# Kernel tuning notes

Hardware: AMD Instinct MI355X
Metric: run time of the kernel (lower is better)

## Reference

```python
import jax, jax.numpy as jnp
import numpy as np

DIM_SINGLE = 384
DIM_PAIR = 128
HEADS = 12
DIM_POINT = 4
B, N = 1, 1024
EPS = 1e-5


def _gram_schmidt_rot(key, shape):
    k1, k2 = jax.random.split(key)
    v1 = jax.random.normal(k1, shape + (3,), jnp.float32)
    v2 = jax.random.normal(k2, shape + (3,), jnp.float32)
    x = v1 / jnp.linalg.norm(v1, axis=-1, keepdims=True)
    z = jnp.cross(x, v2)
    z = z / jnp.linalg.norm(z, axis=-1, keepdims=True)
    y = jnp.cross(z, x)
    # columns are basis vectors, matching torch.stack([x,y,z], dim=-1)
    return jnp.stack([x, y, z], axis=-1)


def setup_inputs() -> dict:
    key = jax.random.key(0)
    ks = jax.random.split(key, 24)
    C, Cp, H, P = DIM_SINGLE, DIM_PAIR, HEADS, DIM_POINT
    HP3 = H * P * 3
    s = lambda k, sh, sc: (jax.random.normal(k, sh, jnp.float32) * sc)
    inp = {
        'single': jax.random.normal(ks[0], (B, N, C), jnp.float32),
        'pair': jax.random.normal(ks[1], (B, N, N, Cp), jnp.float32),
        'rot': _gram_schmidt_rot(ks[2], (B, N)),
        'trans': jax.random.normal(ks[3], (B, N, 3), jnp.float32),
        'mask': jnp.ones((B, N), dtype=bool),
        'Wq': s(ks[4], (C, C), C ** -0.5), 'bq': jnp.zeros((C,), jnp.float32),
        'Wk': s(ks[5], (C, C), C ** -0.5), 'bk': jnp.zeros((C,), jnp.float32),
        'Wv': s(ks[6], (C, C), C ** -0.5), 'bv': jnp.zeros((C,), jnp.float32),
        'Wpb': s(ks[7], (Cp, H), Cp ** -0.5), 'bpb': jnp.zeros((H,), jnp.float32),
        'Wqp': s(ks[8], (C, HP3), C ** -0.5), 'bqp': jnp.zeros((HP3,), jnp.float32),
        'Wkp': s(ks[9], (C, HP3), C ** -0.5), 'bkp': jnp.zeros((HP3,), jnp.float32),
        'Wvp': s(ks[10], (C, HP3), C ** -0.5), 'bvp': jnp.zeros((HP3,), jnp.float32),
        'Wo': s(ks[11], (C, C), C ** -0.5), 'bo': jnp.zeros((C,), jnp.float32),
        'Wpo': s(ks[12], (HP3, C), HP3 ** -0.5), 'bpo': jnp.zeros((C,), jnp.float32),
        'gamma': jnp.ones((C,), jnp.float32), 'beta': jnp.zeros((C,), jnp.float32),
    }
    return inp


def ipa_forward(single, pair, rot, trans, mask,
                Wq, bq, Wk, bk, Wv, bv, Wpb, bpb,
                Wqp, bqp, Wkp, bkp, Wvp, bvp,
                Wo, bo, Wpo, bpo, gamma, beta):
    Bn, Nn, C = single.shape
    H, P = HEADS, DIM_POINT
    Ch = C // H
    scale = Ch ** -0.5

    q = (single @ Wq + bq).reshape(Bn, Nn, H, Ch)
    k = (single @ Wk + bk).reshape(Bn, Nn, H, Ch)
    v = (single @ Wv + bv).reshape(Bn, Nn, H, Ch)

    pair_bias = (pair @ Wpb + bpb).transpose(0, 3, 1, 2)  # [B,H,N,N]

    def pts(W, b):
        p = (single @ W + b).reshape(Bn, Nn, H, P, 3)
        # point as row-vector times rot (matches torch einsum bnhpd,bnhde->bnhpe)
        p = jnp.einsum('bnhpd,bnde->bnhpe', p, rot) + trans[:, :, None, None, :]
        return p

    q_pts = pts(Wqp, bqp)
    k_pts = pts(Wkp, bkp)
    v_pts = pts(Wvp, bvp)

    q2 = jnp.sum(q_pts ** 2, axis=(3, 4))  # [B,N,H]
    k2 = jnp.sum(k_pts ** 2, axis=(3, 4))

    scalar_logits = jnp.einsum('bmhc,bnhc->bhmn', q, k) * scale
    qk_pts = jnp.einsum('bmhpd,bnhpd->bhmn', q_pts, k_pts)
    point_logits = -0.5 * (q2.transpose(0, 2, 1)[:, :, :, None]
                           + k2.transpose(0, 2, 1)[:, :, None, :]
                           - 2.0 * qk_pts) * scale
    logits = scalar_logits + point_logits + pair_bias

    mask2d = mask[:, None, :, None] & mask[:, None, None, :]  # [B,1,M,N]
    logits = jnp.where(mask2d, logits, -1e9)

    attn = jax.nn.softmax(logits, axis=-1)  # [B,H,M,N]

    out_scalar = jnp.einsum('bhmn,bnhc->bmhc', attn, v).reshape(Bn, Nn, C)
    out_points = jnp.einsum('bhmn,bnhpd->bmhpd', attn, v_pts).reshape(Bn, Nn, H * P * 3)

    out = out_scalar @ Wo + bo + out_points @ Wpo + bpo
    x = single + out
    mu = jnp.mean(x, axis=-1, keepdims=True)
    var = jnp.var(x, axis=-1, keepdims=True)
    return (x - mu) / jnp.sqrt(var + EPS) * gamma + beta


def reference(single, pair, rot, trans, mask,
              Wq, bq, Wk, bk, Wv, bv, Wpb, bpb,
              Wqp, bqp, Wkp, bkp, Wvp, bvp,
              Wo, bo, Wpo, bpo, gamma, beta):
    return ipa_forward(single, pair, rot, trans, mask,
                       Wq, bq, Wk, bk, Wv, bv, Wpb, bpb,
                       Wqp, bqp, Wkp, bkp, Wvp, bvp,
                       Wo, bo, Wpo, bpo, gamma, beta)
```

## Files before the change

### kernel.cpp

```cpp
#include <hip/hip_runtime.h>
#include <cmath>


#define SCALE 0.17677669529663687f

#define OFF_QQ 0u
#define OFF_KK 589824u
#define OFF_VV 1179648u
#define OFF_SM 1769472u
#define OFF_SIS 1781760u
#define OFF_OA4 1794048u
#define OFF_OA 3956736u
#define OFF_LG 4497408u
#define OFF_PM 17080320u
#define OFF_PS 17129472u
#define WS_FLOATS 17178624ull

__device__ __forceinline__ void fma4(float4& a, const float4& w, float s) {
  a.x = fmaf(w.x, s, a.x); a.y = fmaf(w.y, s, a.y);
  a.z = fmaf(w.z, s, a.z); a.w = fmaf(w.w, s, a.w);
}

__global__ __launch_bounds__(256) void k_gemm(
    const float* __restrict__ single, const float* __restrict__ rotm,
    const float* __restrict__ trans, const float* __restrict__ bpb,
    const float* __restrict__ Wq, const float* __restrict__ bq,
    const float* __restrict__ Wk, const float* __restrict__ bk,
    const float* __restrict__ Wv, const float* __restrict__ bv,
    const float* __restrict__ Wqp, const float* __restrict__ bqp,
    const float* __restrict__ Wkp, const float* __restrict__ bkp,
    const float* __restrict__ Wvp, const float* __restrict__ bvp,
    float* __restrict__ ws)
{
  __shared__ float sA[64 * 37];
  __shared__ float sB[48 * 37];
  const int tid = threadIdx.x;
  const int m0 = blockIdx.x * 64;
  const int ct = blockIdx.y;
  float* QQ = ws + OFF_QQ; float* KK = ws + OFF_KK; float* VV = ws + OFF_VV;
  const float* W; const float* bb; int OUT, cb, w_;
  if (ct < 24) {
    w_ = ct >> 3;
    W  = w_ == 0 ? Wq : (w_ == 1 ? Wk : Wv);
    bb = w_ == 0 ? bq : (w_ == 1 ? bk : bv);
    OUT = 384; cb = (ct & 7) * 48;
  } else {
    int pt = ct - 24; w_ = pt / 3;
    W  = w_ == 0 ? Wqp : (w_ == 1 ? Wkp : Wvp);
    bb = w_ == 0 ? bqp : (w_ == 1 ? bkp : bvp);
    OUT = 144; cb = (pt - w_ * 3) * 48;
  }
  const int tr = tid >> 4, tc = tid & 15;
  const int r0 = tr * 4;
  const int k4s = tid & 7, mrs = tid >> 3;
  const int c4b = tid % 12, kkb = tid / 12;
  const int f1 = tid + 256;
  const int c4b1 = f1 % 12, kkb1 = f1 / 12;

  float acc[4][3];
  #pragma unroll
  for (int i = 0; i < 4; ++i)
    #pragma unroll
    for (int j = 0; j < 3; ++j) acc[i][j] = 0.f;

  float4 pa0 = *(const float4*)&single[(size_t)(m0 + mrs) * 384 + k4s * 4];
  float4 pa1 = *(const float4*)&single[(size_t)(m0 + mrs + 32) * 384 + k4s * 4];
  float4 pb0 = *(const float4*)&W[(size_t)kkb * OUT + cb + c4b * 4];
  float4 pb1;
  if (tid < 128) pb1 = *(const float4*)&W[(size_t)kkb1 * OUT + cb + c4b1 * 4];

  for (int kc = 0; kc < 12; ++kc) {
    *(float4*)&sA[mrs * 37 + k4s * 4] = pa0;
    *(float4*)&sA[(mrs + 32) * 37 + k4s * 4] = pa1;
    sB[(c4b * 4 + 0) * 37 + kkb] = pb0.x;
    sB[(c4b * 4 + 1) * 37 + kkb] = pb0.y;
    sB[(c4b * 4 + 2) * 37 + kkb] = pb0.z;
    sB[(c4b * 4 + 3) * 37 + kkb] = pb0.w;
    if (tid < 128) {
      sB[(c4b1 * 4 + 0) * 37 + kkb1] = pb1.x;
      sB[(c4b1 * 4 + 1) * 37 + kkb1] = pb1.y;
      sB[(c4b1 * 4 + 2) * 37 + kkb1] = pb1.z;
      sB[(c4b1 * 4 + 3) * 37 + kkb1] = pb1.w;
    }
    if (kc < 11) {
      int kn = (kc + 1) * 32;
      pa0 = *(const float4*)&single[(size_t)(m0 + mrs) * 384 + kn + k4s * 4];
      pa1 = *(const float4*)&single[(size_t)(m0 + mrs + 32) * 384 + kn + k4s * 4];
      pb0 = *(const float4*)&W[(size_t)(kn + kkb) * OUT + cb + c4b * 4];
      if (tid < 128) pb1 = *(const float4*)&W[(size_t)(kn + kkb1) * OUT + cb + c4b1 * 4];
    }
    __syncthreads();
    #pragma unroll
    for (int k4 = 0; k4 < 8; ++k4) {
      float4 av[4], bv_[3];
      #pragma unroll
      for (int i = 0; i < 4; ++i) av[i] = *(const float4*)&sA[(r0 + i) * 37 + k4 * 4];
      #pragma unroll
      for (int j = 0; j < 3; ++j) bv_[j] = *(const float4*)&sB[(tc * 3 + j) * 37 + k4 * 4];
      #pragma unroll
      for (int i = 0; i < 4; ++i)
        #pragma unroll
        for (int j = 0; j < 3; ++j)
          acc[i][j] += av[i].x * bv_[j].x + av[i].y * bv_[j].y
                     + av[i].z * bv_[j].z + av[i].w * bv_[j].w;
    }
    __syncthreads();
  }

  if (ct < 24) {
    #pragma unroll
    for (int i = 0; i < 4; ++i) {
      int m = m0 + r0 + i;
      #pragma unroll
      for (int j = 0; j < 3; ++j) {
        int c = cb + tc * 3 + j;
        float v = acc[i][j] + bb[c];
        int h = c >> 5, cc = c & 31;
        if (w_ == 0)      QQ[h * 49152 + m * 48 + cc] = SCALE * v;
        else if (w_ == 1) KK[h * 49152 + m * 48 + cc] = v;
        else              VV[m * 576 + h * 48 + cc] = v;
      }
    }
  } else {
    const int pe = cb / 3 + tc;
    const int h = pe >> 2, p = pe & 3;
    #pragma unroll
    for (int i = 0; i < 4; ++i) {
      int m = m0 + r0 + i;
      const float* R = rotm + m * 9;
      float raw0 = acc[i][0] + bb[cb + tc * 3 + 0];
      float raw1 = acc[i][1] + bb[cb + tc * 3 + 1];
      float raw2 = acc[i][2] + bb[cb + tc * 3 + 2];
      float v0 = raw0 * R[0] + raw1 * R[3] + raw2 * R[6] + trans[m * 3 + 0];
      float v1 = raw0 * R[1] + raw1 * R[4] + raw2 * R[7] + trans[m * 3 + 1];
      float v2 = raw0 * R[2] + raw1 * R[5] + raw2 * R[8] + trans[m * 3 + 2];
      if (w_ == 2) {
        float* d = VV + m * 576 + h * 48 + 32 + p * 3;
        d[0] = v0; d[1] = v1; d[2] = v2;
      } else {
        float s2 = v0 * v0 + v1 * v1 + v2 * v2;
        s2 += __shfl_xor(s2, 1);
        s2 += __shfl_xor(s2, 2);
        if (w_ == 0) {
          float* d = QQ + h * 49152 + m * 48;
          d[32 + p * 3 + 0] = SCALE * v0;
          d[32 + p * 3 + 1] = SCALE * v1;
          d[32 + p * 3 + 2] = SCALE * v2;
          if (p == 0) {
            d[44] = 1.f; d[45] = -0.5f * SCALE * s2; d[46] = 0.f; d[47] = 0.f;
          }
        } else {
          float* d = KK + h * 49152 + m * 48;
          d[32 + p * 3 + 0] = v0;
          d[32 + p * 3 + 1] = v1;
          d[32 + p * 3 + 2] = v2;
          if (p == 0) {
            d[44] = bpb[h] - 0.5f * SCALE * s2; d[45] = 1.f;
            d[46] = 0.f; d[47] = 0.f;
          }
        }
      }
    }
  }
}

__global__ __launch_bounds__(256) void k_qkdot(const float* __restrict__ QQ,
                                               const float* __restrict__ KK,
                                               float* __restrict__ LG)
{
  __shared__ float sQ[64 * 52];
  __shared__ float sK[128 * 52];
  const int tid = threadIdx.x;
  const int n0 = blockIdx.x * 128, m0 = blockIdx.y * 64, hh = blockIdx.z;
  const float* Qg = QQ + (size_t)hh * 49152 + (size_t)m0 * 48;
  const float* Kg = KK + (size_t)hh * 49152 + (size_t)n0 * 48;
  for (int i = tid; i < 768; i += 256) {
    int r = i / 12, c4 = (i - r * 12) * 4;
    *(float4*)&sQ[r * 52 + c4] = *(const float4*)&Qg[r * 48 + c4];
  }
  for (int i = tid; i < 1536; i += 256) {
    int r = i / 12, c4 = (i - r * 12) * 4;
    *(float4*)&sK[r * 52 + c4] = *(const float4*)&Kg[r * 48 + c4];
  }
  __syncthreads();
  const int mb = (tid >> 4) * 4, nb = tid & 15;
  float acc[4][8];
  #pragma unroll
  for (int i = 0; i < 4; ++i)
    #pragma unroll
    for (int j = 0; j < 8; ++j) acc[i][j] = 0.f;
  #pragma unroll
  for (int j4 = 0; j4 < 48; j4 += 4) {
    float4 q[4], k[8];
    #pragma unroll
    for (int i = 0; i < 4; ++i) q[i] = *(const float4*)&sQ[(mb + i) * 52 + j4];
    #pragma unroll
    for (int j = 0; j < 8; ++j) k[j] = *(const float4*)&sK[(nb + j * 16) * 52 + j4];
    #pragma unroll
    for (int i = 0; i < 4; ++i)
      #pragma unroll
      for (int j = 0; j < 8; ++j)
        acc[i][j] += q[i].x * k[j].x + q[i].y * k[j].y + q[i].z * k[j].z + q[i].w * k[j].w;
  }
  float* Lb = LG + (size_t)hh * 1048576 + (size_t)m0 * 1024 + n0;
  #pragma unroll
  for (int i = 0; i < 4; ++i)
    #pragma unroll
    for (int j = 0; j < 8; ++j)
      Lb[(mb + i) * 1024 + nb + j * 16] = acc[i][j];
}

__global__ __launch_bounds__(256) void k_bias(const float* __restrict__ pair,
                                              const float* __restrict__ Wpb,
                                              float* __restrict__ LG,
                                              float* __restrict__ PM,
                                              float* __restrict__ PS)
{
  __shared__ float sP[256 * 33];
  __shared__ float sRed[4][12];
  __shared__ float sRed2[4][12];
  const int tid = threadIdx.x;
  const size_t base = (size_t)blockIdx.x * 256;
  const int c4 = tid & 7, r8 = tid >> 3;
  float acc[12];
  #pragma unroll
  for (int h = 0; h < 12; ++h) acc[h] = 0.f;

  float4 pre[8];
  #pragma unroll
  for (int k = 0; k < 8; ++k)
    pre[k] = *(const float4*)&pair[(base + k * 32 + r8) * 128 + c4 * 4];

  for (int cc = 0; cc < 4; ++cc) {
    #pragma unroll
    for (int k = 0; k < 8; ++k) {
      float* d = &sP[(k * 32 + r8) * 33 + c4 * 4];
      d[0] = pre[k].x; d[1] = pre[k].y; d[2] = pre[k].z; d[3] = pre[k].w;
    }
    if (cc < 3) {
      #pragma unroll
      for (int k = 0; k < 8; ++k)
        pre[k] = *(const float4*)&pair[(base + k * 32 + r8) * 128 + (cc + 1) * 32 + c4 * 4];
    }
    __syncthreads();
    const float* rp = &sP[tid * 33];
    #pragma unroll 8
    for (int j = 0; j < 32; ++j) {
      float p = rp[j];
      const float* w = Wpb + (cc * 32 + j) * 12;
      #pragma unroll
      for (int h = 0; h < 12; ++h) acc[h] = fmaf(p, w[h], acc[h]);
    }
    __syncthreads();
  }
  float lf[12];
  float* L = LG + base + tid;
  #pragma unroll
  for (int h = 0; h < 12; ++h) {
    lf[h] = L[(size_t)h * 1048576] + acc[h];
    L[(size_t)h * 1048576] = lf[h];
  }
  const int lane = tid & 63, wv = tid >> 6;
  #pragma unroll
  for (int h = 0; h < 12; ++h) {
    float mx = lf[h];
    #pragma unroll
    for (int d = 32; d; d >>= 1) mx = fmaxf(mx, __shfl_xor(mx, d));
    if (lane == 0) sRed[wv][h] = mx;
  }
  __syncthreads();
  float Mq[12];
  #pragma unroll
  for (int h = 0; h < 12; ++h)
    Mq[h] = fmaxf(fmaxf(sRed[0][h], sRed[1][h]), fmaxf(sRed[2][h], sRed[3][h]));
  #pragma unroll
  for (int h = 0; h < 12; ++h) {
    float se = __expf(lf[h] - Mq[h]);
    #pragma unroll
    for (int d = 32; d; d >>= 1) se += __shfl_xor(se, d);
    if (lane == 0) sRed2[wv][h] = se;
  }
  __syncthreads();
  if (tid < 12) {
    float S = sRed2[0][tid] + sRed2[1][tid] + sRed2[2][tid] + sRed2[3][tid];
    int m = blockIdx.x >> 2, q = blockIdx.x & 3;
    PM[tid * 4096 + m * 4 + q] = Mq[tid];
    PS[tid * 4096 + m * 4 + q] = S;
  }
}

__global__ __launch_bounds__(256) void k_mstats(const float* __restrict__ PM,
                                                const float* __restrict__ PS,
                                                float* __restrict__ SM,
                                                float* __restrict__ SIS)
{
  int idx = blockIdx.x * 256 + threadIdx.x;
  if (idx >= 12288) return;
  int b = idx * 4;
  float m0 = PM[b], m1 = PM[b + 1], m2 = PM[b + 2], m3 = PM[b + 3];
  float M = fmaxf(fmaxf(m0, m1), fmaxf(m2, m3));
  float S = PS[b] * __expf(m0 - M) + PS[b + 1] * __expf(m1 - M)
          + PS[b + 2] * __expf(m2 - M) + PS[b + 3] * __expf(m3 - M);
  SM[idx] = M;
  SIS[idx] = 1.f / S;
}

__global__ __launch_bounds__(256) void k_av(const float* __restrict__ LG,
                                            const float* __restrict__ VV,
                                            const float* __restrict__ SM,
                                            float* __restrict__ OA4)
{
  __shared__ float sA[64 * 68];
  __shared__ float sBt[48 * 68];
  __shared__ float sMl[64];
  const int tid = threadIdx.x;
  const int m0 = blockIdx.x * 64, n0 = blockIdx.y * 256, hh = blockIdx.z;
  const int q = blockIdx.y;
  const float* Lh = LG + (size_t)hh * 1048576;
  const int mi4 = tid >> 4, cj3 = tid & 15;

  if (tid < 64) sMl[tid] = SM[hh * 1024 + m0 + tid];
  for (int i = tid; i < 4 * 68; i += 256) sBt[44 * 68 + i] = 0.f;
  __syncthreads();

  float acc[4][3];
  #pragma unroll
  for (int i = 0; i < 4; ++i)
    #pragma unroll
    for (int j = 0; j < 3; ++j) acc[i][j] = 0.f;

  for (int kc = 0; kc < 4; ++kc) {
    const int nb = n0 + kc * 64;
    #pragma unroll
    for (int t = 0; t < 4; ++t) {
      int idx = tid + t * 256;
      int row = idx >> 4, c4 = idx & 15;
      float4 x = *(const float4*)&Lh[(size_t)(m0 + row) * 1024 + nb + c4 * 4];
      float mrow = sMl[row];
      float4 e;
      e.x = __expf(x.x - mrow); e.y = __expf(x.y - mrow);
      e.z = __expf(x.z - mrow); e.w = __expf(x.w - mrow);
      *(float4*)&sA[row * 68 + c4 * 4] = e;
    }
    for (int idx = tid; idx < 704; idx += 256) {
      int r = idx / 11, c4 = idx - r * 11;
      float4 v = *(const float4*)&VV[(size_t)(nb + r) * 576 + hh * 48 + c4 * 4];
      sBt[(c4 * 4 + 0) * 68 + r] = v.x;
      sBt[(c4 * 4 + 1) * 68 + r] = v.y;
      sBt[(c4 * 4 + 2) * 68 + r] = v.z;
      sBt[(c4 * 4 + 3) * 68 + r] = v.w;
    }
    __syncthreads();
    #pragma unroll 4
    for (int k4 = 0; k4 < 16; ++k4) {
      float4 a0 = *(const float4*)&sA[(mi4 * 4 + 0) * 68 + k4 * 4];
      float4 a1 = *(const float4*)&sA[(mi4 * 4 + 1) * 68 + k4 * 4];
      float4 a2 = *(const float4*)&sA[(mi4 * 4 + 2) * 68 + k4 * 4];
      float4 a3 = *(const float4*)&sA[(mi4 * 4 + 3) * 68 + k4 * 4];
      float4 b0 = *(const float4*)&sBt[(cj3 * 3 + 0) * 68 + k4 * 4];
      float4 b1 = *(const float4*)&sBt[(cj3 * 3 + 1) * 68 + k4 * 4];
      float4 b2 = *(const float4*)&sBt[(cj3 * 3 + 2) * 68 + k4 * 4];
      acc[0][0] += a0.x*b0.x + a0.y*b0.y + a0.z*b0.z + a0.w*b0.w;
      acc[0][1] += a0.x*b1.x + a0.y*b1.y + a0.z*b1.z + a0.w*b1.w;
      acc[0][2] += a0.x*b2.x + a0.y*b2.y + a0.z*b2.z + a0.w*b2.w;
      acc[1][0] += a1.x*b0.x + a1.y*b0.y + a1.z*b0.z + a1.w*b0.w;
      acc[1][1] += a1.x*b1.x + a1.y*b1.y + a1.z*b1.z + a1.w*b1.w;
      acc[1][2] += a1.x*b2.x + a1.y*b2.y + a1.z*b2.z + a1.w*b2.w;
      acc[2][0] += a2.x*b0.x + a2.y*b0.y + a2.z*b0.z + a2.w*b0.w;
      acc[2][1] += a2.x*b1.x + a2.y*b1.y + a2.z*b1.z + a2.w*b1.w;
      acc[2][2] += a2.x*b2.x + a2.y*b2.y + a2.z*b2.z + a2.w*b2.w;
      acc[3][0] += a3.x*b0.x + a3.y*b0.y + a3.z*b0.z + a3.w*b0.w;
      acc[3][1] += a3.x*b1.x + a3.y*b1.y + a3.z*b1.z + a3.w*b1.w;
      acc[3][2] += a3.x*b2.x + a3.y*b2.y + a3.z*b2.z + a3.w*b2.w;
    }
    __syncthreads();
  }
  #pragma unroll
  for (int i = 0; i < 4; ++i)
    #pragma unroll
    for (int j = 0; j < 3; ++j) {
      int c = cj3 * 3 + j;
      if (c < 44)
        OA4[(size_t)q * 540672 + (size_t)(m0 + mi4 * 4 + i) * 528 + hh * 44 + c]
            = acc[i][j];
    }
}

__global__ __launch_bounds__(256) void k_merge(const float* __restrict__ OA4,
                                               const float* __restrict__ SIS,
                                               float* __restrict__ OA)
{
  int idx = blockIdx.x * 256 + threadIdx.x;
  if (idx >= 540672) return;
  int m = idx / 528, c = idx - m * 528;
  int h = c / 44;
  float v = OA4[idx] + OA4[540672 + idx] + OA4[2 * 540672 + idx]
          + OA4[3 * 540672 + idx];
  OA[idx] = v * SIS[h * 1024 + m];
}

__global__ __launch_bounds__(128) void k_final(
    const float* __restrict__ OA, const float* __restrict__ single,
    const float* __restrict__ Wo, const float* __restrict__ bo,
    const float* __restrict__ Wpo, const float* __restrict__ bpo,
    const float* __restrict__ gamma, const float* __restrict__ beta,
    float* __restrict__ out)
{
  __shared__ float sX[2 * 384];
  const int tid = threadIdx.x;
  const int m0 = blockIdx.x * 2;
  if (tid < 96) {
    int o4 = tid * 4;
    float4 b1 = *(const float4*)&bo[o4];
    float4 b2 = *(const float4*)&bpo[o4];
    float4 bs = make_float4(b1.x + b2.x, b1.y + b2.y, b1.z + b2.z, b1.w + b2.w);
    float4 acc[2] = {bs, bs};
    const float* oab = OA + (size_t)m0 * 528;
    #pragma unroll 1
    for (int hh = 0; hh < 12; ++hh) {
      #pragma unroll
      for (int j4 = 0; j4 < 8; ++j4) {
        const float* wp = Wo + (size_t)(hh * 32 + j4 * 4) * 384 + o4;
        float4 w0 = *(const float4*)(wp);
        float4 w1 = *(const float4*)(wp + 384);
        float4 w2 = *(const float4*)(wp + 768);
        float4 w3 = *(const float4*)(wp + 1152);
        #pragma unroll
        for (int mi = 0; mi < 2; ++mi) {
          float4 s = *(const float4*)(oab + mi * 528 + hh * 44 + j4 * 4);
          fma4(acc[mi], w0, s.x); fma4(acc[mi], w1, s.y);
          fma4(acc[mi], w2, s.z); fma4(acc[mi], w3, s.w);
        }
      }
      #pragma unroll
      for (int j4 = 0; j4 < 3; ++j4) {
        const float* wp = Wpo + (size_t)(hh * 12 + j4 * 4) * 384 + o4;
        float4 w0 = *(const float4*)(wp);
        float4 w1 = *(const float4*)(wp + 384);
        float4 w2 = *(const float4*)(wp + 768);
        float4 w3 = *(const float4*)(wp + 1152);
        #pragma unroll
        for (int mi = 0; mi < 2; ++mi) {
          float4 s = *(const float4*)(oab + mi * 528 + hh * 44 + 32 + j4 * 4);
          fma4(acc[mi], w0, s.x); fma4(acc[mi], w1, s.y);
          fma4(acc[mi], w2, s.z); fma4(acc[mi], w3, s.w);
        }
      }
    }
    #pragma unroll
    for (int mi = 0; mi < 2; ++mi) {
      float4 sg = *(const float4*)&single[(size_t)(m0 + mi) * 384 + o4];
      float4 x = make_float4(acc[mi].x + sg.x, acc[mi].y + sg.y,
                             acc[mi].z + sg.z, acc[mi].w + sg.w);
      *(float4*)&sX[mi * 384 + o4] = x;
    }
  }
  __syncthreads();
  const int lane = tid & 63, r = tid >> 6;
  float xs[6]; float s = 0.f;
  #pragma unroll
  for (int i = 0; i < 6; ++i) { xs[i] = sX[r * 384 + lane * 6 + i]; s += xs[i]; }
  #pragma unroll
  for (int d = 32; d; d >>= 1) s += __shfl_xor(s, d);
  float mu = s * (1.f / 384.f);
  float vs = 0.f;
  #pragma unroll
  for (int i = 0; i < 6; ++i) { float dd = xs[i] - mu; vs = fmaf(dd, dd, vs); }
  #pragma unroll
  for (int d = 32; d; d >>= 1) vs += __shfl_xor(vs, d);
  float rstd = rsqrtf(vs * (1.f / 384.f) + 1e-5f);
  #pragma unroll
  for (int i = 0; i < 6; ++i) {
    int c = lane * 6 + i;
    out[(size_t)(m0 + r) * 384 + c] = (xs[i] - mu) * rstd * gamma[c] + beta[c];
  }
}

__global__ void k_wsfail(float* out, int n) {
  int i = blockIdx.x * 256 + threadIdx.x;
  if (i < n) out[i] = 12345.0f;
}

extern "C" void kernel_launch(void* const* d_in, const int* in_sizes, int n_in,
                              void* d_out, int out_size, void* d_ws, size_t ws_size,
                              hipStream_t stream)
{
  (void)in_sizes; (void)n_in;
  const float* single = (const float*)d_in[0];
  const float* pair   = (const float*)d_in[1];
  const float* rotm   = (const float*)d_in[2];
  const float* trans  = (const float*)d_in[3];
  const float* Wq  = (const float*)d_in[5];
  const float* bq  = (const float*)d_in[6];
  const float* Wk  = (const float*)d_in[7];
  const float* bk  = (const float*)d_in[8];
  const float* Wv  = (const float*)d_in[9];
  const float* bv  = (const float*)d_in[10];
  const float* Wpb = (const float*)d_in[11];
  const float* bpb = (const float*)d_in[12];
  const float* Wqp = (const float*)d_in[13];
  const float* bqp = (const float*)d_in[14];
  const float* Wkp = (const float*)d_in[15];
  const float* bkp = (const float*)d_in[16];
  const float* Wvp = (const float*)d_in[17];
  const float* bvp = (const float*)d_in[18];
  const float* Wo  = (const float*)d_in[19];
  const float* bo  = (const float*)d_in[20];
  const float* Wpo = (const float*)d_in[21];
  const float* bpo = (const float*)d_in[22];
  const float* gamma = (const float*)d_in[23];
  const float* beta  = (const float*)d_in[24];
  float* ws  = (float*)d_ws;
  float* out = (float*)d_out;

  if (ws_size < WS_FLOATS * 4ull) {
    k_wsfail<<<(out_size + 255) / 256, 256, 0, stream>>>(out, out_size);
    return;
  }

  k_gemm<<<dim3(16, 33), 256, 0, stream>>>(single, rotm, trans, bpb,
      Wq, bq, Wk, bk, Wv, bv, Wqp, bqp, Wkp, bkp, Wvp, bvp, ws);
  k_qkdot<<<dim3(8, 16, 12), 256, 0, stream>>>(ws + OFF_QQ, ws + OFF_KK,
                                               ws + OFF_LG);
  k_bias<<<4096, 256, 0, stream>>>(pair, Wpb, ws + OFF_LG, ws + OFF_PM,
                                   ws + OFF_PS);
  k_mstats<<<48, 256, 0, stream>>>(ws + OFF_PM, ws + OFF_PS, ws + OFF_SM,
                                   ws + OFF_SIS);
  k_av<<<dim3(16, 4, 12), 256, 0, stream>>>(ws + OFF_LG, ws + OFF_VV,
                                            ws + OFF_SM, ws + OFF_OA4);
  k_merge<<<2112, 256, 0, stream>>>(ws + OFF_OA4, ws + OFF_SIS, ws + OFF_OA);
  k_final<<<512, 128, 0, stream>>>(ws + OFF_OA, single, Wo, bo, Wpo, bpo,
                                   gamma, beta, out);
}
```

Measured before the change: 309.5 us.

## Fuse QK logit dot product into pair-bias kernel with transposed K layout

Removes the separate k_qkdot kernel and computes the per-(m,n,h) query-key dot product (scalar plus point terms) inside k_bias, which already touches every logit. K is now stored transposed (feature-major, n contiguous), so each thread reads coalesced K columns while the block's query row sits in shared memory. This avoids writing the logits tensor and reading it back. In exchange, k_bias does 44 extra global K loads per head per thread with no register-tiled reuse across m, which leans on L2 for the K tensor.

```diff
diff --git a/kernel.cpp b/kernel.cpp
--- a/kernel.cpp
+++ b/kernel.cpp
@@ -5,7 +5,7 @@
 #define SCALE 0.17677669529663687f
 
 #define OFF_QQ 0u
-#define OFF_KK 589824u
+#define OFF_KKT 589824u
 #define OFF_VV 1179648u
 #define OFF_SM 1769472u
 #define OFF_SIS 1781760u
@@ -37,7 +37,7 @@
   const int tid = threadIdx.x;
   const int m0 = blockIdx.x * 64;
   const int ct = blockIdx.y;
-  float* QQ = ws + OFF_QQ; float* KK = ws + OFF_KK; float* VV = ws + OFF_VV;
+  float* QQ = ws + OFF_QQ; float* KKT = ws + OFF_KKT; float* VV = ws + OFF_VV;
   const float* W; const float* bb; int OUT, cb, w_;
   if (ct < 24) {
     w_ = ct >> 3;
@@ -117,7 +117,7 @@
         float v = acc[i][j] + bb[c];
         int h = c >> 5, cc = c & 31;
         if (w_ == 0)      QQ[h * 49152 + m * 48 + cc] = SCALE * v;
-        else if (w_ == 1) KK[h * 49152 + m * 48 + cc] = v;
+        else if (w_ == 1) KKT[(size_t)(h * 45 + cc) * 1024 + m] = v;
         else              VV[m * 576 + h * 48 + cc] = v;
       }
     }
@@ -150,86 +150,46 @@
             d[44] = 1.f; d[45] = -0.5f * SCALE * s2; d[46] = 0.f; d[47] = 0.f;
           }
         } else {
-          float* d = KK + h * 49152 + m * 48;
-          d[32 + p * 3 + 0] = v0;
-          d[32 + p * 3 + 1] = v1;
-          d[32 + p * 3 + 2] = v2;
-          if (p == 0) {
-            d[44] = bpb[h] - 0.5f * SCALE * s2; d[45] = 1.f;
-            d[46] = 0.f; d[47] = 0.f;
-          }
+          float* d = KKT + (size_t)(h * 45 + 32 + p * 3) * 1024 + m;
+          d[0] = v0; d[1024] = v1; d[2048] = v2;
+          if (p == 0)
+            KKT[(size_t)(h * 45 + 44) * 1024 + m] = bpb[h] - 0.5f * SCALE * s2;
         }
       }
     }
   }
 }
 
-__global__ __launch_bounds__(256) void k_qkdot(const float* __restrict__ QQ,
-                                               const float* __restrict__ KK,
-                                               float* __restrict__ LG)
-{
-  __shared__ float sQ[64 * 52];
-  __shared__ float sK[128 * 52];
-  const int tid = threadIdx.x;
-  const int n0 = blockIdx.x * 128, m0 = blockIdx.y * 64, hh = blockIdx.z;
-  const float* Qg = QQ + (size_t)hh * 49152 + (size_t)m0 * 48;
-  const float* Kg = KK + (size_t)hh * 49152 + (size_t)n0 * 48;
-  for (int i = tid; i < 768; i += 256) {
-    int r = i / 12, c4 = (i - r * 12) * 4;
-    *(float4*)&sQ[r * 52 + c4] = *(const float4*)&Qg[r * 48 + c4];
-  }
-  for (int i = tid; i < 1536; i += 256) {
-    int r = i / 12, c4 = (i - r * 12) * 4;
-    *(float4*)&sK[r * 52 + c4] = *(const float4*)&Kg[r * 48 + c4];
-  }
-  __syncthreads();
-  const int mb = (tid >> 4) * 4, nb = tid & 15;
-  float acc[4][8];
-  #pragma unroll
-  for (int i = 0; i < 4; ++i)
-    #pragma unroll
-    for (int j = 0; j < 8; ++j) acc[i][j] = 0.f;
-  #pragma unroll
-  for (int j4 = 0; j4 < 48; j4 += 4) {
-    float4 q[4], k[8];
-    #pragma unroll
-    for (int i = 0; i < 4; ++i) q[i] = *(const float4*)&sQ[(mb + i) * 52 + j4];
-    #pragma unroll
-    for (int j = 0; j < 8; ++j) k[j] = *(const float4*)&sK[(nb + j * 16) * 52 + j4];
-    #pragma unroll
-    for (int i = 0; i < 4; ++i)
-      #pragma unroll
-      for (int j = 0; j < 8; ++j)
-        acc[i][j] += q[i].x * k[j].x + q[i].y * k[j].y + q[i].z * k[j].z + q[i].w * k[j].w;
-  }
-  float* Lb = LG + (size_t)hh * 1048576 + (size_t)m0 * 1024 + n0;
-  #pragma unroll
-  for (int i = 0; i < 4; ++i)
-    #pragma unroll
-    for (int j = 0; j < 8; ++j)
-      Lb[(mb + i) * 1024 + nb + j * 16] = acc[i][j];
-}
-
 __global__ __launch_bounds__(256) void k_bias(const float* __restrict__ pair,
                                               const float* __restrict__ Wpb,
+                                              const float* __restrict__ KKT,
+                                              const float* __restrict__ QQ,
                                               float* __restrict__ LG,
                                               float* __restrict__ PM,
                                               float* __restrict__ PS)
 {
   __shared__ float sP[256 * 33];
+  __shared__ float sQ[576];
   __shared__ float sRed[4][12];
   __shared__ float sRed2[4][12];
   const int tid = threadIdx.x;
   const size_t base = (size_t)blockIdx.x * 256;
+  const int m = blockIdx.x >> 2;
+  const int nn = ((blockIdx.x & 3) << 8) | tid;
   const int c4 = tid & 7, r8 = tid >> 3;
   float acc[12];
   #pragma unroll
   for (int h = 0; h < 12; ++h) acc[h] = 0.f;
 
+  if (tid < 144) {
+    int h = tid / 12, q4 = (tid - h * 12) * 4;
+    *(float4*)&sQ[h * 48 + q4] = *(const float4*)&QQ[h * 49152 + m * 48 + q4];
+  }
   float4 pre[8];
   #pragma unroll
   for (int k = 0; k < 8; ++k)
     pre[k] = *(const float4*)&pair[(base + k * 32 + r8) * 128 + c4 * 4];
+  __syncthreads();
 
   for (int cc = 0; cc < 4; ++cc) {
     #pragma unroll
@@ -251,13 +211,29 @@
       #pragma unroll
       for (int h = 0; h < 12; ++h) acc[h] = fmaf(p, w[h], acc[h]);
     }
+    #pragma unroll
+    for (int r = 0; r < 3; ++r) {
+      const int h = cc * 3 + r;
+      const float* kb = KKT + (size_t)(h * 45) * 1024 + nn;
+      const float* qb = &sQ[h * 48];
+      float t0 = kb[44 * 1024] + qb[45];
+      float t1 = 0.f, t2 = 0.f, t3 = 0.f;
+      #pragma unroll
+      for (int j = 0; j < 44; j += 4) {
+        t0 = fmaf(qb[j + 0], kb[(j + 0) * 1024], t0);
+        t1 = fmaf(qb[j + 1], kb[(j + 1) * 1024], t1);
+        t2 = fmaf(qb[j + 2], kb[(j + 2) * 1024], t2);
+        t3 = fmaf(qb[j + 3], kb[(j + 3) * 1024], t3);
+      }
+      acc[h] += (t0 + t1) + (t2 + t3);
+    }
     __syncthreads();
   }
   float lf[12];
   float* L = LG + base + tid;
   #pragma unroll
   for (int h = 0; h < 12; ++h) {
-    lf[h] = L[(size_t)h * 1048576] + acc[h];
+    lf[h] = acc[h];
     L[(size_t)h * 1048576] = lf[h];
   }
   const int lane = tid & 63, wv = tid >> 6;
@@ -283,9 +259,9 @@
   __syncthreads();
   if (tid < 12) {
     float S = sRed2[0][tid] + sRed2[1][tid] + sRed2[2][tid] + sRed2[3][tid];
-    int m = blockIdx.x >> 2, q = blockIdx.x & 3;
-    PM[tid * 4096 + m * 4 + q] = Mq[tid];
-    PS[tid * 4096 + m * 4 + q] = S;
+    int mm = blockIdx.x >> 2, q = blockIdx.x & 3;
+    PM[tid * 4096 + mm * 4 + q] = Mq[tid];
+    PS[tid * 4096 + mm * 4 + q] = S;
   }
 }
 
@@ -520,10 +496,8 @@
 
   k_gemm<<<dim3(16, 33), 256, 0, stream>>>(single, rotm, trans, bpb,
       Wq, bq, Wk, bk, Wv, bv, Wqp, bqp, Wkp, bkp, Wvp, bvp, ws);
-  k_qkdot<<<dim3(8, 16, 12), 256, 0, stream>>>(ws + OFF_QQ, ws + OFF_KK,
-                                               ws + OFF_LG);
-  k_bias<<<4096, 256, 0, stream>>>(pair, Wpb, ws + OFF_LG, ws + OFF_PM,
-                                   ws + OFF_PS);
+  k_bias<<<4096, 256, 0, stream>>>(pair, Wpb, ws + OFF_KKT, ws + OFF_QQ,
+                                   ws + OFF_LG, ws + OFF_PM, ws + OFF_PS);
   k_mstats<<<48, 256, 0, stream>>>(ws + OFF_PM, ws + OFF_PS, ws + OFF_SM,
                                    ws + OFF_SIS);
   k_av<<<dim3(16, 4, 12), 256, 0, stream>>>(ws + OFF_LG, ws + OFF_VV,
```

Result: slower. 336.2 us (+8.6%).
